# Kernel optimization log

Hardware: AMD Instinct MI355X
Metric: run time of the kernel (lower is better)

Reference implementation:

```python
import jax, jax.numpy as jnp
import numpy as np

N = 50000      # nodes per graph
E = 1600000    # edges per graph
D_IN = 128
D_HID = 128
D_OUT = 128
D_GF = 128
N_LAYERS = 3   # input->hid, hid->hid (hidden_layer=1), hid->out


def setup_inputs() -> dict:
    key = jax.random.key(0)
    ks = jax.random.split(key, 24)
    inp = {
        "feat_p": jax.random.normal(ks[0], (N, D_IN), jnp.float32),
        "src_p": jax.random.randint(ks[1], (E,), 0, N, jnp.int32),
        "dst_p": jax.random.randint(ks[2], (E,), 0, N, jnp.int32),
        "feat_s": jax.random.normal(ks[3], (N, D_IN), jnp.float32),
        "src_s": jax.random.randint(ks[4], (E,), 0, N, jnp.int32),
        "dst_s": jax.random.randint(ks[5], (E,), 0, N, jnp.int32),
    }
    dims = [(D_IN, D_HID), (D_HID, D_HID), (D_HID, D_OUT)]
    for i, (di, do) in enumerate(dims):
        inp[f"W{i}"] = jax.random.normal(ks[6 + 2 * i], (di, do), jnp.float32) * 0.05
        inp[f"b{i}"] = jnp.zeros((do,), jnp.float32)
    inp["Wr"] = jax.random.normal(ks[14], (D_OUT, D_GF), jnp.float32) * 0.05
    inp["br"] = jnp.zeros((D_GF,), jnp.float32)
    inp["Wm1"] = jax.random.normal(ks[15], (2 * D_GF, D_GF), jnp.float32) * 0.05
    inp["bm1"] = jnp.zeros((D_GF,), jnp.float32)
    inp["Wm2"] = jax.random.normal(ks[16], (D_GF, 1), jnp.float32) * 0.05
    inp["bm2"] = jnp.zeros((1,), jnp.float32)
    return inp


def _gcn_stack(feat, src, dst, layers):
    """Stacked GCN: mean over incoming messages, then linear.
    NOTE: the original SingleGCN never applies its ReLU (bug preserved)."""
    n = feat.shape[0]
    deg = jax.ops.segment_sum(jnp.ones_like(src, feat.dtype), dst, num_segments=n)
    inv_deg = (1.0 / jnp.maximum(deg, 1.0))[:, None]  # [N,1]
    h = feat
    for W, b in layers:
        msg = h[src]                                           # [E,d] gather
        agg = jax.ops.segment_sum(msg, dst, num_segments=n)    # [N,d] scatter-add
        h = (agg * inv_deg) @ W + b                            # mean + linear
    return h


def reference(feat_p, src_p, dst_p, feat_s, src_s, dst_s,
              W0, b0, W1, b1, W2, b2, Wr, br, Wm1, bm1, Wm2, bm2):
    layers = [(W0, b0), (W1, b1), (W2, b2)]
    h_p = _gcn_stack(feat_p, src_p, dst_p, layers)
    h_s = _gcn_stack(feat_s, src_s, dst_s, layers)
    # ReadOut: mean over nodes -> linear -> sigmoid
    g_p = jax.nn.sigmoid(jnp.mean(h_p, axis=0) @ Wr + br)  # [D_GF]
    g_s = jax.nn.sigmoid(jnp.mean(h_s, axis=0) @ Wr + br)
    # Match: concat -> linear -> linear -> sigmoid
    c = jnp.concatenate([g_p, g_s], axis=-1)               # [2*D_GF]
    d = (c @ Wm1 + bm1) @ Wm2 + bm2                        # [1]
    return jax.nn.sigmoid(d)
```

## Files before the change

kernel.cpp:

```cpp
#include <hip/hip_runtime.h>
#include <math.h>

#define D 128


__global__ __launch_bounds__(256) void scan_scatter(
        const int* __restrict__ tgt_p, const int* __restrict__ oth_p,
        const int* __restrict__ tgt_s, const int* __restrict__ oth_s,
        const float* __restrict__ w, float* __restrict__ rep,
        int E, int N, int HN, int B, int H, float scale) {
    const int b = blockIdx.x, h = blockIdx.y, g = blockIdx.z;
    const int* tgt = g ? tgt_s : tgt_p;
    const int* oth = g ? oth_s : oth_p;
    const float* wg = w ? (w + (size_t)g * N) : nullptr;

    extern __shared__ float lds[];
    {
        float4 z = make_float4(0.f, 0.f, 0.f, 0.f);
        float4* l4 = (float4*)lds;
        for (int i = threadIdx.x; i < HN / 4; i += blockDim.x) l4[i] = z;
    }
    __syncthreads();

    const int lo = h * HN;
    const int hi = min(lo + HN, N);
    const unsigned span = (unsigned)(hi - lo);
    int C = (E + B - 1) / B;
    C = (C + 15) & ~15;
    const int e0 = b * C;
    const int e1 = min(e0 + C, E);

    for (int e = e0 + (int)threadIdx.x * 16; e < e1; e += blockDim.x * 16) {
        if (e + 16 <= e1) {
            int idx[16];
            #pragma unroll
            for (int q = 0; q < 4; ++q) {
                int4 t4 = *(const int4*)(tgt + e + 4 * q);
                idx[4 * q + 0] = t4.x; idx[4 * q + 1] = t4.y;
                idx[4 * q + 2] = t4.z; idx[4 * q + 3] = t4.w;
            }
            bool hit[16];
            #pragma unroll
            for (int k = 0; k < 16; ++k) hit[k] = (unsigned)(idx[k] - lo) < span;
            if (wg) {
                int od[16];
                #pragma unroll
                for (int q = 0; q < 4; ++q) {
                    int4 o4 = *(const int4*)(oth + e + 4 * q);
                    od[4 * q + 0] = o4.x; od[4 * q + 1] = o4.y;
                    od[4 * q + 2] = o4.z; od[4 * q + 3] = o4.w;
                }
                float val[16];
                #pragma unroll
                for (int k = 0; k < 16; ++k) val[k] = hit[k] ? wg[od[k]] : 0.f;
                #pragma unroll
                for (int k = 0; k < 16; ++k)
                    if (hit[k]) atomicAdd(&lds[idx[k] - lo], val[k] * scale);
            } else {
                #pragma unroll
                for (int k = 0; k < 16; ++k)
                    if (hit[k]) atomicAdd(&lds[idx[k] - lo], 1.0f);
            }
        } else {
            for (int e2 = e; e2 < e1; ++e2) {
                int t = tgt[e2];
                if ((unsigned)(t - lo) < span) {
                    float v = wg ? wg[oth[e2]] * scale : 1.0f;
                    atomicAdd(&lds[t - lo], v);
                }
            }
        }
    }
    __syncthreads();

    float* dst = rep + (((size_t)g * H + h) * B + b) * HN;
    float4* d4 = (float4*)dst;
    const float4* l4 = (const float4*)lds;
    for (int i = threadIdx.x; i < HN / 4; i += blockDim.x) d4[i] = l4[i];
}

__global__ void reduce_inv(const float* __restrict__ rep, float* __restrict__ inv,
                           int N, int HN, int H, int B) {
    int i = blockIdx.x * blockDim.x + threadIdx.x;
    if (i >= 2 * N) return;
    int g = (i < N) ? 0 : 1;
    int n = i - g * N;
    int h = n / HN, l = n - h * HN;
    const float* base = rep + (((size_t)g * H + h) * B) * HN + l;
    float s = 0.f;
    #pragma unroll 16
    for (int b = 0; b < B; b++) s += base[(size_t)b * HN];
    inv[i] = 1.0f / fmaxf(s, 1.0f);
}

__global__ void reduce_u(const float* __restrict__ rep, const float* __restrict__ inv,
                         float* __restrict__ out_u, float* __restrict__ out_w,
                         float* __restrict__ sums, int s_idx,
                         int N, int HN, int H, int B) {
    int i = blockIdx.x * blockDim.x + threadIdx.x;
    float u = 0.f;
    if (i < 2 * N) {
        int g = (i < N) ? 0 : 1;
        int n = i - g * N;
        int h = n / HN, l = n - h * HN;
        const float* base = rep + (((size_t)g * H + h) * B) * HN + l;
        #pragma unroll 16
        for (int b = 0; b < B; b++) u += base[(size_t)b * HN];
        if (out_u) out_u[i] = u;
        if (out_w) out_w[i] = u * inv[i];
    }
    if (sums) {
        __shared__ float sm0[256], sm1[256];
        sm0[threadIdx.x] = (i < N) ? u : 0.f;
        sm1[threadIdx.x] = (i >= N && i < 2 * N) ? u : 0.f;
        __syncthreads();
        for (int s = 128; s > 0; s >>= 1) {
            if ((int)threadIdx.x < s) {
                sm0[threadIdx.x] += sm0[threadIdx.x + s];
                sm1[threadIdx.x] += sm1[threadIdx.x + s];
            }
            __syncthreads();
        }
        if (threadIdx.x == 0) {
            if (sm0[0] != 0.f) atomicAdd(&sums[0 * 2 + s_idx], sm0[0]);
            if (sm1[0] != 0.f) atomicAdd(&sums[1 * 2 + s_idx], sm1[0]);
        }
    }
}

__global__ __launch_bounds__(256) void featsum_kernel(
        const float* __restrict__ feat_p, const float* __restrict__ feat_s,
        const float* __restrict__ u3, float* __restrict__ fpart, int N) {
    const int g = blockIdx.y;
    const float* feat = g ? feat_s : feat_p;
    const float* u = u3 + (size_t)g * N;
    const int nb = gridDim.x;
    const int col4 = threadIdx.x & 31;
    const int rgrp = threadIdx.x >> 5;
    const int rows_per_block = (N + nb - 1) / nb;
    const int r0 = blockIdx.x * rows_per_block;
    const int r1 = min(r0 + rows_per_block, N);

    const float4* f4 = (const float4*)feat;
    float4 acc = make_float4(0.f, 0.f, 0.f, 0.f);
    for (int n = r0 + rgrp; n < r1; n += 8) {
        float wv = u[n];
        float4 v = f4[(size_t)n * 32 + col4];
        acc.x += wv * v.x; acc.y += wv * v.y; acc.z += wv * v.z; acc.w += wv * v.w;
    }
    __shared__ float4 smem[256];
    smem[threadIdx.x] = acc;
    __syncthreads();
    if (rgrp == 0) {
        float4 t = smem[col4];
        #pragma unroll
        for (int k = 1; k < 8; k++) {
            float4 o = smem[k * 32 + col4];
            t.x += o.x; t.y += o.y; t.z += o.z; t.w += o.w;
        }
        float4* dst = (float4*)(fpart + ((size_t)g * nb + blockIdx.x) * 128);
        dst[col4] = t;
    }
}

__global__ void final_kernel(const float* __restrict__ fpart, int NB,
                             const float* __restrict__ sums,
                             const float* __restrict__ W0, const float* __restrict__ b0,
                             const float* __restrict__ W1, const float* __restrict__ b1,
                             const float* __restrict__ W2, const float* __restrict__ b2,
                             const float* __restrict__ Wr, const float* __restrict__ br,
                             const float* __restrict__ Wm1, const float* __restrict__ bm1,
                             const float* __restrict__ Wm2, const float* __restrict__ bm2,
                             float* __restrict__ out) {
    __shared__ float t[128];
    __shared__ float c[256];
    const int j = threadIdx.x;

    for (int g = 0; g < 2; ++g) {
        const float s1 = sums[g * 2 + 0];
        const float s2 = sums[g * 2 + 1];
        float rv = 0.f;
        const float* fp = fpart + (size_t)g * NB * 128 + j;
        #pragma unroll 16
        for (int b = 0; b < NB; ++b) rv += fp[(size_t)b * 128];
        t[j] = rv;
        __syncthreads();
        float v = s2 * b0[j];
        for (int i = 0; i < 128; ++i) v += t[i] * W0[i * 128 + j];
        __syncthreads(); t[j] = v; __syncthreads();
        v = s1 * b1[j];
        for (int i = 0; i < 128; ++i) v += t[i] * W1[i * 128 + j];
        __syncthreads(); t[j] = v; __syncthreads();
        v = b2[j];
        for (int i = 0; i < 128; ++i) v += t[i] * W2[i * 128 + j];
        __syncthreads(); t[j] = v; __syncthreads();
        v = br[j];
        for (int i = 0; i < 128; ++i) v += t[i] * Wr[i * 128 + j];
        c[g * 128 + j] = 1.0f / (1.0f + expf(-v));
        __syncthreads();
    }

    float v = bm1[j];
    for (int i = 0; i < 256; ++i) v += c[i] * Wm1[i * 128 + j];
    t[j] = v * Wm2[j];
    __syncthreads();
    if (j == 0) {
        float d = bm2[0];
        for (int i = 0; i < 128; ++i) d += t[i];
        out[0] = 1.0f / (1.0f + expf(-d));
    }
}

extern "C" void kernel_launch(void* const* d_in, const int* in_sizes, int n_in,
                              void* d_out, int out_size, void* d_ws, size_t ws_size,
                              hipStream_t stream) {
    const float* feat_p = (const float*)d_in[0];
    const int*   src_p  = (const int*)d_in[1];
    const int*   dst_p  = (const int*)d_in[2];
    const float* feat_s = (const float*)d_in[3];
    const int*   src_s  = (const int*)d_in[4];
    const int*   dst_s  = (const int*)d_in[5];
    const float* W0 = (const float*)d_in[6];
    const float* b0 = (const float*)d_in[7];
    const float* W1 = (const float*)d_in[8];
    const float* b1 = (const float*)d_in[9];
    const float* W2 = (const float*)d_in[10];
    const float* b2 = (const float*)d_in[11];
    const float* Wr = (const float*)d_in[12];
    const float* br = (const float*)d_in[13];
    const float* Wm1 = (const float*)d_in[14];
    const float* bm1 = (const float*)d_in[15];
    const float* Wm2 = (const float*)d_in[16];
    const float* bm2 = (const float*)d_in[17];
    float* out = (float*)d_out;

    const int N = in_sizes[0] / D;
    const int E = in_sizes[1];
    const int N2 = 2 * N;

    const int H = 4;
    int HN = (N + H - 1) / H;
    HN = (HN + 3) & ~3;
    const int NB = 384;

    const size_t head = 16 + 4 * (size_t)N2 + (size_t)2 * NB * 128;
    size_t avail = ws_size / sizeof(float);
    int B = 8;
    if (avail > head) {
        size_t bmax = (avail - head) / ((size_t)2 * H * HN);
        if (bmax > 96) bmax = 96;
        B = (int)(bmax & ~(size_t)7);
        if (B < 1) B = 1;
    } else {
        B = 1;
    }

    float* ws    = (float*)d_ws;
    float* sums  = ws;
    float* inv   = ws + 16;
    float* w1    = inv + N2;
    float* w2    = w1 + N2;
    float* u3    = w2 + N2;
    float* fpart = u3 + N2;
    float* rep   = fpart + (size_t)2 * NB * 128;

    hipMemsetAsync(d_ws, 0, 16 * sizeof(float), stream);

    const int BT = 256;
    const dim3 sgrid(B, H, 2);
    const size_t lds_bytes = (size_t)HN * sizeof(float);
    const int gN2 = (N2 + BT - 1) / BT;
    const float u0 = 1.0f / (float)N;

    scan_scatter<<<sgrid, BT, lds_bytes, stream>>>(dst_p, nullptr, dst_s, nullptr,
                                                   nullptr, rep, E, N, HN, B, H, 1.0f);
    reduce_inv<<<gN2, BT, 0, stream>>>(rep, inv, N, HN, H, B);

    scan_scatter<<<sgrid, BT, lds_bytes, stream>>>(src_p, dst_p, src_s, dst_s,
                                                   inv, rep, E, N, HN, B, H, u0);
    reduce_u<<<gN2, BT, 0, stream>>>(rep, inv, nullptr, w1, sums, 0, N, HN, H, B);

    scan_scatter<<<sgrid, BT, lds_bytes, stream>>>(src_p, dst_p, src_s, dst_s,
                                                   w1, rep, E, N, HN, B, H, 1.0f);
    reduce_u<<<gN2, BT, 0, stream>>>(rep, inv, nullptr, w2, sums, 1, N, HN, H, B);

    scan_scatter<<<sgrid, BT, lds_bytes, stream>>>(src_p, dst_p, src_s, dst_s,
                                                   w2, rep, E, N, HN, B, H, 1.0f);
    reduce_u<<<gN2, BT, 0, stream>>>(rep, inv, u3, nullptr, nullptr, 0, N, HN, H, B);

    featsum_kernel<<<dim3(NB, 2), BT, 0, stream>>>(feat_p, feat_s, u3, fpart, N);

    final_kernel<<<1, 128, 0, stream>>>(fpart, NB, sums, W0, b0, W1, b1, W2, b2,
                                        Wr, br, Wm1, bm1, Wm2, bm2, out);
}
```

Baseline: 334.5 us.

## Vectorize reductions, unroll featsum, parallelize final kernel, double featsum blocks

The reduce kernels now have each thread handle four nodes with float4 loads and stores. The featsum loop is unrolled four-way so more loads are in flight, and its block count is doubled. The final kernel runs with 512 threads, splitting each matvec four ways and precomputing the bias-propagation vectors. Together these target the small-kernel tail and the under-parallel single-block final stage. The float4 paths assume N and HN are multiples of 4 so that vectors never straddle graph or partition boundaries.

```diff
diff --git a/kernel.cpp b/kernel.cpp
--- a/kernel.cpp
+++ b/kernel.cpp
@@ -81,38 +81,54 @@
 
 __global__ void reduce_inv(const float* __restrict__ rep, float* __restrict__ inv,
                            int N, int HN, int H, int B) {
-    int i = blockIdx.x * blockDim.x + threadIdx.x;
+    int i = (blockIdx.x * blockDim.x + threadIdx.x) * 4;
     if (i >= 2 * N) return;
     int g = (i < N) ? 0 : 1;
     int n = i - g * N;
     int h = n / HN, l = n - h * HN;
     const float* base = rep + (((size_t)g * H + h) * B) * HN + l;
-    float s = 0.f;
+    float4 s = make_float4(0.f, 0.f, 0.f, 0.f);
     #pragma unroll 16
-    for (int b = 0; b < B; b++) s += base[(size_t)b * HN];
-    inv[i] = 1.0f / fmaxf(s, 1.0f);
+    for (int b = 0; b < B; b++) {
+        float4 v = *(const float4*)(base + (size_t)b * HN);
+        s.x += v.x; s.y += v.y; s.z += v.z; s.w += v.w;
+    }
+    float4 r;
+    r.x = 1.0f / fmaxf(s.x, 1.0f); r.y = 1.0f / fmaxf(s.y, 1.0f);
+    r.z = 1.0f / fmaxf(s.z, 1.0f); r.w = 1.0f / fmaxf(s.w, 1.0f);
+    *(float4*)(inv + i) = r;
 }
 
 __global__ void reduce_u(const float* __restrict__ rep, const float* __restrict__ inv,
                          float* __restrict__ out_u, float* __restrict__ out_w,
                          float* __restrict__ sums, int s_idx,
                          int N, int HN, int H, int B) {
-    int i = blockIdx.x * blockDim.x + threadIdx.x;
-    float u = 0.f;
+    int i = (blockIdx.x * blockDim.x + threadIdx.x) * 4;
+    float tp = 0.f, ts = 0.f;
     if (i < 2 * N) {
         int g = (i < N) ? 0 : 1;
         int n = i - g * N;
         int h = n / HN, l = n - h * HN;
         const float* base = rep + (((size_t)g * H + h) * B) * HN + l;
+        float4 u = make_float4(0.f, 0.f, 0.f, 0.f);
         #pragma unroll 16
-        for (int b = 0; b < B; b++) u += base[(size_t)b * HN];
-        if (out_u) out_u[i] = u;
-        if (out_w) out_w[i] = u * inv[i];
+        for (int b = 0; b < B; b++) {
+            float4 v = *(const float4*)(base + (size_t)b * HN);
+            u.x += v.x; u.y += v.y; u.z += v.z; u.w += v.w;
+        }
+        if (out_u) *(float4*)(out_u + i) = u;
+        if (out_w) {
+            float4 iv = *(const float4*)(inv + i);
+            float4 wv = make_float4(u.x * iv.x, u.y * iv.y, u.z * iv.z, u.w * iv.w);
+            *(float4*)(out_w + i) = wv;
+        }
+        float t = u.x + u.y + u.z + u.w;
+        if (g == 0) tp = t; else ts = t;
     }
     if (sums) {
         __shared__ float sm0[256], sm1[256];
-        sm0[threadIdx.x] = (i < N) ? u : 0.f;
-        sm1[threadIdx.x] = (i >= N && i < 2 * N) ? u : 0.f;
+        sm0[threadIdx.x] = tp;
+        sm1[threadIdx.x] = ts;
         __syncthreads();
         for (int s = 128; s > 0; s >>= 1) {
             if ((int)threadIdx.x < s) {
@@ -143,7 +159,19 @@
 
     const float4* f4 = (const float4*)feat;
     float4 acc = make_float4(0.f, 0.f, 0.f, 0.f);
-    for (int n = r0 + rgrp; n < r1; n += 8) {
+    int n = r0 + rgrp;
+    for (; n + 24 < r1; n += 32) {
+        float w0 = u[n], w1 = u[n + 8], w2 = u[n + 16], w3 = u[n + 24];
+        float4 v0 = f4[(size_t)n * 32 + col4];
+        float4 v1 = f4[(size_t)(n + 8) * 32 + col4];
+        float4 v2 = f4[(size_t)(n + 16) * 32 + col4];
+        float4 v3 = f4[(size_t)(n + 24) * 32 + col4];
+        acc.x += w0 * v0.x + w1 * v1.x + w2 * v2.x + w3 * v3.x;
+        acc.y += w0 * v0.y + w1 * v1.y + w2 * v2.y + w3 * v3.y;
+        acc.z += w0 * v0.z + w1 * v1.z + w2 * v2.z + w3 * v3.z;
+        acc.w += w0 * v0.w + w1 * v1.w + w2 * v2.w + w3 * v3.w;
+    }
+    for (; n < r1; n += 8) {
         float wv = u[n];
         float4 v = f4[(size_t)n * 32 + col4];
         acc.x += wv * v.x; acc.y += wv * v.y; acc.z += wv * v.z; acc.w += wv * v.w;
@@ -163,51 +191,98 @@
     }
 }
 
-__global__ void final_kernel(const float* __restrict__ fpart, int NB,
-                             const float* __restrict__ sums,
-                             const float* __restrict__ W0, const float* __restrict__ b0,
-                             const float* __restrict__ W1, const float* __restrict__ b1,
-                             const float* __restrict__ W2, const float* __restrict__ b2,
-                             const float* __restrict__ Wr, const float* __restrict__ br,
-                             const float* __restrict__ Wm1, const float* __restrict__ bm1,
-                             const float* __restrict__ Wm2, const float* __restrict__ bm2,
-                             float* __restrict__ out) {
-    __shared__ float t[128];
-    __shared__ float c[256];
-    const int j = threadIdx.x;
+__global__ __launch_bounds__(512) void final_kernel(
+        const float* __restrict__ fpart, int NB,
+        const float* __restrict__ sums,
+        const float* __restrict__ W0, const float* __restrict__ b0,
+        const float* __restrict__ W1, const float* __restrict__ b1,
+        const float* __restrict__ W2, const float* __restrict__ b2,
+        const float* __restrict__ Wr, const float* __restrict__ br,
+        const float* __restrict__ Wm1, const float* __restrict__ bm1,
+        const float* __restrict__ Wm2, const float* __restrict__ bm2,
+        float* __restrict__ out) {
+    __shared__ float x[128];
+    __shared__ float part[4][128];
+    __shared__ float rvec[256];
+    __shared__ float Avec[128], Bvec[128];
+    __shared__ float gv[256];
+    const int tid = threadIdx.x;
+    const int j = tid & 127;
+    const int h = tid >> 7;
+
+    auto mv128 = [&](const float* __restrict__ W, float* __restrict__ buf) {
+        float p = 0.f;
+        const float* Wp = W + (size_t)(h * 32) * 128 + j;
+        #pragma unroll
+        for (int i = 0; i < 32; ++i) p += buf[h * 32 + i] * Wp[(size_t)i * 128];
+        part[h][j] = p;
+        __syncthreads();
+        if (h == 0) buf[j] = part[0][j] + part[1][j] + part[2][j] + part[3][j];
+        __syncthreads();
+    };
+
+    const int nb4 = NB / 4;
+    for (int g = 0; g < 2; ++g) {
+        const float* fp = fpart + (size_t)(g * NB + h * nb4) * 128 + j;
+        float p = 0.f;
+        #pragma unroll 16
+        for (int b = 0; b < nb4; ++b) p += fp[(size_t)b * 128];
+        part[h][j] = p;
+        __syncthreads();
+        if (h == 0) rvec[g * 128 + j] = part[0][j] + part[1][j] + part[2][j] + part[3][j];
+        __syncthreads();
+    }
+
+    if (tid < 128) x[tid] = b0[tid];
+    __syncthreads();
+    mv128(W1, x);
+    mv128(W2, x);
+    if (tid < 128) Avec[tid] = x[tid];
+    __syncthreads();
+    if (tid < 128) x[tid] = b1[tid];
+    __syncthreads();
+    mv128(W2, x);
+    if (tid < 128) Bvec[tid] = x[tid];
+    __syncthreads();
 
     for (int g = 0; g < 2; ++g) {
         const float s1 = sums[g * 2 + 0];
         const float s2 = sums[g * 2 + 1];
-        float rv = 0.f;
-        const float* fp = fpart + (size_t)g * NB * 128 + j;
-        #pragma unroll 16
-        for (int b = 0; b < NB; ++b) rv += fp[(size_t)b * 128];
-        t[j] = rv;
-        __syncthreads();
-        float v = s2 * b0[j];
-        for (int i = 0; i < 128; ++i) v += t[i] * W0[i * 128 + j];
-        __syncthreads(); t[j] = v; __syncthreads();
-        v = s1 * b1[j];
-        for (int i = 0; i < 128; ++i) v += t[i] * W1[i * 128 + j];
-        __syncthreads(); t[j] = v; __syncthreads();
-        v = b2[j];
-        for (int i = 0; i < 128; ++i) v += t[i] * W2[i * 128 + j];
-        __syncthreads(); t[j] = v; __syncthreads();
-        v = br[j];
-        for (int i = 0; i < 128; ++i) v += t[i] * Wr[i * 128 + j];
-        c[g * 128 + j] = 1.0f / (1.0f + expf(-v));
-        __syncthreads();
-    }
-
-    float v = bm1[j];
-    for (int i = 0; i < 256; ++i) v += c[i] * Wm1[i * 128 + j];
-    t[j] = v * Wm2[j];
-    __syncthreads();
-    if (j == 0) {
-        float d = bm2[0];
-        for (int i = 0; i < 128; ++i) d += t[i];
-        out[0] = 1.0f / (1.0f + expf(-d));
+        if (tid < 128) x[tid] = rvec[g * 128 + tid];
+        __syncthreads();
+        mv128(W0, x);
+        mv128(W1, x);
+        mv128(W2, x);
+        if (tid < 128) x[tid] += s2 * Avec[tid] + s1 * Bvec[tid] + b2[tid];
+        __syncthreads();
+        mv128(Wr, x);
+        if (tid < 128) gv[g * 128 + tid] = 1.0f / (1.0f + expf(-(x[tid] + br[tid])));
+        __syncthreads();
+    }
+
+    {
+        float p = 0.f;
+        const float* Wp = Wm1 + (size_t)(h * 64) * 128 + j;
+        #pragma unroll
+        for (int i = 0; i < 64; ++i) p += gv[h * 64 + i] * Wp[(size_t)i * 128];
+        part[h][j] = p;
+        __syncthreads();
+        if (h == 0)
+            part[0][j] = (part[0][j] + part[1][j] + part[2][j] + part[3][j] + bm1[j]) * Wm2[j];
+        __syncthreads();
+        if (tid < 64) part[0][tid] += part[0][tid + 64];
+        __syncthreads();
+        if (tid < 32) part[0][tid] += part[0][tid + 32];
+        __syncthreads();
+        if (tid < 16) part[0][tid] += part[0][tid + 16];
+        __syncthreads();
+        if (tid < 8) part[0][tid] += part[0][tid + 8];
+        __syncthreads();
+        if (tid < 4) part[0][tid] += part[0][tid + 4];
+        __syncthreads();
+        if (tid < 2) part[0][tid] += part[0][tid + 2];
+        __syncthreads();
+        if (tid == 0) out[0] = 1.0f / (1.0f + expf(-(part[0][0] + part[0][1] + bm2[0])));
     }
 }
 
@@ -241,7 +316,7 @@
     const int H = 4;
     int HN = (N + H - 1) / H;
     HN = (HN + 3) & ~3;
-    const int NB = 384;
+    const int NB = 768;
 
     const size_t head = 16 + 4 * (size_t)N2 + (size_t)2 * NB * 128;
     size_t avail = ws_size / sizeof(float);
@@ -269,27 +344,27 @@
     const int BT = 256;
     const dim3 sgrid(B, H, 2);
     const size_t lds_bytes = (size_t)HN * sizeof(float);
-    const int gN2 = (N2 + BT - 1) / BT;
+    const int gQ = (N2 / 4 + BT - 1) / BT;
     const float u0 = 1.0f / (float)N;
 
     scan_scatter<<<sgrid, BT, lds_bytes, stream>>>(dst_p, nullptr, dst_s, nullptr,
                                                    nullptr, rep, E, N, HN, B, H, 1.0f);
-    reduce_inv<<<gN2, BT, 0, stream>>>(rep, inv, N, HN, H, B);
+    reduce_inv<<<gQ, BT, 0, stream>>>(rep, inv, N, HN, H, B);
 
     scan_scatter<<<sgrid, BT, lds_bytes, stream>>>(src_p, dst_p, src_s, dst_s,
                                                    inv, rep, E, N, HN, B, H, u0);
-    reduce_u<<<gN2, BT, 0, stream>>>(rep, inv, nullptr, w1, sums, 0, N, HN, H, B);
+    reduce_u<<<gQ, BT, 0, stream>>>(rep, inv, nullptr, w1, sums, 0, N, HN, H, B);
 
     scan_scatter<<<sgrid, BT, lds_bytes, stream>>>(src_p, dst_p, src_s, dst_s,
                                                    w1, rep, E, N, HN, B, H, 1.0f);
-    reduce_u<<<gN2, BT, 0, stream>>>(rep, inv, nullptr, w2, sums, 1, N, HN, H, B);
+    reduce_u<<<gQ, BT, 0, stream>>>(rep, inv, nullptr, w2, sums, 1, N, HN, H, B);
 
     scan_scatter<<<sgrid, BT, lds_bytes, stream>>>(src_p, dst_p, src_s, dst_s,
                                                    w2, rep, E, N, HN, B, H, 1.0f);
-    reduce_u<<<gN2, BT, 0, stream>>>(rep, inv, u3, nullptr, nullptr, 0, N, HN, H, B);
+    reduce_u<<<gQ, BT, 0, stream>>>(rep, inv, u3, nullptr, nullptr, 0, N, HN, H, B);
 
     featsum_kernel<<<dim3(NB, 2), BT, 0, stream>>>(feat_p, feat_s, u3, fpart, N);
 
-    final_kernel<<<1, 128, 0, stream>>>(fpart, NB, sums, W0, b0, W1, b1, W2, b2,
+    final_kernel<<<1, 512, 0, stream>>>(fpart, NB, sums, W0, b0, W1, b1, W2, b2,
                                         Wr, br, Wm1, bm1, Wm2, bm2, out);
 }
```

New measurement: 311.6 us. 1.07x faster.
